# Kernel optimization log

Measured on AMD Instinct MI355X. Metric: run time of the kernel, lower is better.

Reference implementation:

```python
import jax, jax.numpy as jnp
import numpy as np

H = 512  # hidden_dim


def setup_inputs() -> dict:
    key = jax.random.key(0)
    ks = jax.random.split(key, 16)
    inp = {
        "state": jax.random.normal(ks[0], (64,), jnp.float32),
        "p_action": jax.random.normal(ks[1], (4,), jnp.float32),
        "p_reward": jax.random.normal(ks[2], (1,), jnp.float32),
        "timestep": jax.random.normal(ks[3], (1,), jnp.float32),
        "cue": jax.random.normal(ks[4], (H,), jnp.float32),
        "mem_keys": jax.random.normal(ks[5], (100000, H), jnp.float32),
        "mem_vals": jax.random.normal(ks[6], (100000, H), jnp.float32),
        "Wx": jax.random.normal(ks[7], (5 * H, 70), jnp.float32) * 0.05,
        "Wh": jax.random.normal(ks[8], (5 * H, H), jnp.float32) * 0.05,
        "b": jax.random.normal(ks[9], (5 * H,), jnp.float32) * 0.05,
        "actor_w": jax.random.normal(ks[10], (4, H), jnp.float32) * 0.01,
        "actor_b": jnp.zeros((4,), jnp.float32),
        "critic_w": jax.random.normal(ks[11], (1, H), jnp.float32),
        "critic_b": jnp.zeros((1,), jnp.float32),
        "h0": jax.random.normal(ks[12], (H,), jnp.float32),
        "c0": jax.random.normal(ks[13], (H,), jnp.float32),
    }
    return inp


def reference(state, p_action, p_reward, timestep, cue, mem_keys, mem_vals,
              Wx, Wh, b, actor_w, actor_b, critic_w, critic_b, h0, c0):
    # ---- DND.get_memory: l2-kernel softmax-weighted read over memory bank ----
    # sims[n] = -||K[n] - cue||^2 ; m_t = softmax(sims) @ V
    sims = -jnp.sum((mem_keys - cue[None, :]) ** 2, axis=1)  # [N]
    w = jax.nn.softmax(sims)                                  # [N]
    m_t = w @ mem_vals                                        # [H]

    # ---- EpLSTMCell (DND-LSTM cell: gates f,i,o,r + candidate) ----
    x_t = jnp.concatenate([state, p_action, p_reward, timestep])  # [70]
    preact = Wx @ x_t + Wh @ h0 + b                               # [5H]
    gates = jax.nn.sigmoid(preact[: 4 * H])
    f_t, i_t, o_t, r_t = jnp.split(gates, 4)
    c_hat = jnp.tanh(preact[4 * H:])
    c_t = f_t * c0 + i_t * c_hat + r_t * m_t
    h_t = o_t * jnp.tanh(c_t)

    # ---- actor / critic heads ----
    action_dist = jax.nn.softmax(actor_w @ h_t + actor_b)
    value_estimate = critic_w @ h_t + critic_b
    return (action_dist, value_estimate, h_t, c_t)
```

## Files before the change

kernel.cpp:

```cpp
#include <hip/hip_runtime.h>
#include <math.h>

#define HDIM 512
#define NROWS 100000
#define NBLK_A 2048
#define K_CAP 1024

constexpr int SIMS_OFF   = 0;
constexpr int BMIN_OFF   = NROWS;
constexpr int CNTL_OFF   = BMIN_OFF + NBLK_A;
constexpr int CAND_OFF   = CNTL_OFF + NBLK_A;
constexpr int PREACT_OFF = CAND_OFF + NBLK_A * 128;

__device__ __forceinline__ float wave_sum(float v) {
    #pragma unroll
    for (int off = 32; off; off >>= 1) v += __shfl_xor(v, off);
    return v;
}
__device__ __forceinline__ float wave_min(float v) {
    #pragma unroll
    for (int off = 32; off; off >>= 1) v = fminf(v, __shfl_xor(v, off));
    return v;
}
__device__ __forceinline__ float d2sum(float4 a, float4 c) {
    float d, s;
    d = a.x - c.x; s  = d * d;
    d = a.y - c.y; s += d * d;
    d = a.z - c.z; s += d * d;
    d = a.w - c.w; s += d * d;
    return s;
}

__global__ __launch_bounds__(256)
void kA(const float* __restrict__ state, const float* __restrict__ pa,
        const float* __restrict__ pr, const float* __restrict__ ts,
        const float* __restrict__ cue, const float* __restrict__ K,
        const float* __restrict__ Wx, const float* __restrict__ Wh,
        const float* __restrict__ b, const float* __restrict__ h0,
        float* __restrict__ ws) {
    const int lane = threadIdx.x & 63;
    const int wib  = threadIdx.x >> 6;
    const int gw   = blockIdx.x * 4 + wib;
    const int nw   = NBLK_A * 4;

    if (gw < 5 * HDIM) {
        const int row = gw;
        float x0 = state[lane];
        float x1 = 0.f;
        if      (lane < 4)  x1 = pa[lane];
        else if (lane == 4) x1 = pr[0];
        else if (lane == 5) x1 = ts[0];

        const float4* h04 = (const float4*)h0;
        const float4  hA = h04[lane], hB = h04[64 + lane];
        const float4* wh4 = (const float4*)(Wh + (size_t)row * HDIM);
        const float4 a0 = wh4[lane], a1 = wh4[64 + lane];
        float acc = a0.x*hA.x + a0.y*hA.y + a0.z*hA.z + a0.w*hA.w
                  + a1.x*hB.x + a1.y*hB.y + a1.z*hB.z + a1.w*hB.w;
        const float* wxr = Wx + (size_t)row * 70;
        acc += wxr[lane] * x0;
        if (lane < 6) acc += wxr[64 + lane] * x1;
        acc = wave_sum(acc);
        if (lane == 0) ws[PREACT_OFF + row] = acc + b[row];
    }

    const float4* c4 = (const float4*)cue;
    const float4 cA = c4[lane], cB = c4[64 + lane];
    float minss = INFINITY;

    const float4 inf4 = make_float4(INFINITY, INFINITY, INFINITY, INFINITY);
    float4 r0 = inf4, r1 = inf4, r2 = inf4, r3 = inf4;
    int it = 0;

    const int NG = NROWS / 4;
    for (int g = gw; g < NG; g += nw) {
        const int n = g * 4;
        const float* r = K + (size_t)n * HDIM;
        const float4* p0 = (const float4*)(r);
        const float4* p1 = (const float4*)(r + HDIM);
        const float4* p2 = (const float4*)(r + 2 * HDIM);
        const float4* p3 = (const float4*)(r + 3 * HDIM);
        const float4 a0 = p0[lane], b0 = p0[64 + lane];
        const float4 a1 = p1[lane], b1 = p1[64 + lane];
        const float4 a2 = p2[lane], b2 = p2[64 + lane];
        const float4 a3 = p3[lane], b3 = p3[64 + lane];
        float s0 = d2sum(a0, cA) + d2sum(b0, cB);
        float s1 = d2sum(a1, cA) + d2sum(b1, cB);
        float s2 = d2sum(a2, cA) + d2sum(b2, cB);
        float s3 = d2sum(a3, cA) + d2sum(b3, cB);
        #pragma unroll
        for (int off = 32; off; off >>= 1) {
            s0 += __shfl_xor(s0, off);
            s1 += __shfl_xor(s1, off);
            s2 += __shfl_xor(s2, off);
            s3 += __shfl_xor(s3, off);
        }
        if (lane == 0) {
            *(float4*)&ws[SIMS_OFF + n] = make_float4(-s0, -s1, -s2, -s3);
        }
        const float4 res = make_float4(s0, s1, s2, s3);
        if      (it == 0) r0 = res;
        else if (it == 1) r1 = res;
        else if (it == 2) r2 = res;
        else              r3 = res;
        ++it;
        minss = fminf(fminf(minss, s0), fminf(fminf(s1, s2), s3));
    }

    minss = wave_min(minss);
    __shared__ float smin[4];
    __shared__ int   wcnt[4];
    if (lane == 0) smin[wib] = minss;
    __syncthreads();
    const float bminv = fminf(fminf(smin[0], smin[1]),
                              fminf(smin[2], smin[3]));
    if (threadIdx.x == 0) ws[BMIN_OFF + blockIdx.x] = bminv;
    const float thr = bminv + 30.0f;

    const int qi = lane >> 2, qj = lane & 3;
    const float4 rq = (qi == 0) ? r0 : (qi == 1) ? r1 : (qi == 2) ? r2 : r3;
    const float v  = (qj == 0) ? rq.x : (qj == 1) ? rq.y : (qj == 2) ? rq.z : rq.w;
    const bool valid = (lane < 16) && (gw + qi * nw < NG);
    const bool ok    = valid && (v <= thr);
    const unsigned long long mask = __ballot(ok);
    const int cnt = (int)__popcll(mask);
    if (lane == 0) wcnt[wib] = cnt;
    __syncthreads();
    int woff = 0;
    #pragma unroll
    for (int w = 0; w < 4; w++) if (w < wib) woff += wcnt[w];
    if (ok) {
        const int pos = (int)__popcll(mask & ((1ull << lane) - 1ull));
        const int row = (gw + qi * nw) * 4 + qj;
        float2* cand = (float2*)(ws + CAND_OFF);
        cand[(blockIdx.x << 6) + woff + pos] = make_float2(v, __int_as_float(row));
    }
    if (threadIdx.x == 0)
        ((int*)ws)[CNTL_OFF + blockIdx.x] = wcnt[0] + wcnt[1] + wcnt[2] + wcnt[3];
}

__global__ __launch_bounds__(1024)
void kB(const float* __restrict__ V, const float* __restrict__ c0,
        const float* __restrict__ aw, const float* __restrict__ ab,
        const float* __restrict__ cw, const float* __restrict__ cb,
        float* __restrict__ ws, float* __restrict__ out) {
    const int t    = threadIdx.x;
    const int lane = t & 63;
    const int wib  = t >> 6;

    __shared__ float sred[16];
    __shared__ int   wtot[16];
    __shared__ int   stot;
    __shared__ float surv_s[K_CAP];
    __shared__ int   surv_n[K_CAP];
    __shared__ float sden;
    __shared__ float hl[HDIM];
    __shared__ float logits[4];

    float mn = fminf(ws[BMIN_OFF + t], ws[BMIN_OFF + 1024 + t]);
    mn = wave_min(mn);
    if (lane == 0) sred[wib] = mn;
    __syncthreads();
    float smin = sred[0];
    #pragma unroll
    for (int w = 1; w < 16; w++) smin = fminf(smin, sred[w]);
    const float thr = smin + 30.0f;

    const int*    cnts = (const int*)ws + CNTL_OFF;
    const float2* cand = (const float2*)(ws + CAND_OFF);

    int mycnt = 0;
    #pragma unroll
    for (int L = 0; L < 2; L++) {
        const int bidx = 2 * t + L;
        const int c = cnts[bidx];
        for (int e = 0; e < c; e++)
            if (cand[(bidx << 6) + e].x <= thr) mycnt++;
    }
    int inc = mycnt;
    #pragma unroll
    for (int off = 1; off < 64; off <<= 1) {
        const int v = __shfl_up(inc, off);
        if (lane >= off) inc += v;
    }
    if (lane == 63) wtot[wib] = inc;
    __syncthreads();
    int base = 0;
    #pragma unroll
    for (int w = 0; w < 16; w++) if (w < wib) base += wtot[w];
    int off = base + inc - mycnt;
    #pragma unroll
    for (int L = 0; L < 2; L++) {
        const int bidx = 2 * t + L;
        const int c = cnts[bidx];
        for (int e = 0; e < c; e++) {
            const float2 ce = cand[(bidx << 6) + e];
            if (ce.x <= thr) {
                if (off < K_CAP) {
                    surv_s[off] = ce.x;
                    surv_n[off] = __float_as_int(ce.y);
                }
                off++;
            }
        }
    }
    if (t == 1023) stot = off;
    __syncthreads();
    const int tot = (stot < K_CAP) ? stot : K_CAP;

    if (t == 0) {
        float den = 0.f;
        for (int i = 0; i < tot; i++) {
            const float e = expf(smin - surv_s[i]);
            surv_s[i] = e;
            den += e;
        }
        sden = den;
    }
    __syncthreads();
    const float inv_den = 1.f / sden;

    if (t < HDIM) {
        float m = 0.f;
        for (int i = 0; i < tot; i++)
            m += surv_s[i] * V[(size_t)surv_n[i] * HDIM + t];
        m *= inv_den;

        const float pf = ws[PREACT_OFF + t];
        const float pi = ws[PREACT_OFF + HDIM + t];
        const float po = ws[PREACT_OFF + 2*HDIM + t];
        const float prg= ws[PREACT_OFF + 3*HDIM + t];
        const float pc = ws[PREACT_OFF + 4*HDIM + t];
        const float f_t = 1.f / (1.f + expf(-pf));
        const float i_t = 1.f / (1.f + expf(-pi));
        const float o_t = 1.f / (1.f + expf(-po));
        const float r_t = 1.f / (1.f + expf(-prg));
        const float chat = tanhf(pc);
        const float ct = f_t * c0[t] + i_t * chat + r_t * m;
        const float ht = o_t * tanhf(ct);
        out[517 + t] = ct;
        out[5 + t]   = ht;
        hl[t] = ht;
    }
    __syncthreads();

    if (wib < 4) {
        float acc = 0.f;
        #pragma unroll
        for (int j = 0; j < HDIM; j += 64)
            acc += aw[wib * HDIM + j + lane] * hl[j + lane];
        acc = wave_sum(acc);
        if (lane == 0) logits[wib] = acc + ab[wib];
    }
    if (wib == 4) {
        float acc = 0.f;
        #pragma unroll
        for (int j = 0; j < HDIM; j += 64)
            acc += cw[j + lane] * hl[j + lane];
        acc = wave_sum(acc);
        if (lane == 0) out[4] = acc + cb[0];
    }
    __syncthreads();

    if (t == 0) {
        const float mx = fmaxf(fmaxf(logits[0], logits[1]),
                               fmaxf(logits[2], logits[3]));
        const float e0 = expf(logits[0] - mx), e1 = expf(logits[1] - mx);
        const float e2 = expf(logits[2] - mx), e3 = expf(logits[3] - mx);
        const float inv = 1.f / (e0 + e1 + e2 + e3);
        out[0] = e0 * inv; out[1] = e1 * inv;
        out[2] = e2 * inv; out[3] = e3 * inv;
    }
}

extern "C" void kernel_launch(void* const* d_in, const int* in_sizes, int n_in,
                              void* d_out, int out_size, void* d_ws, size_t ws_size,
                              hipStream_t stream) {
    const float* state  = (const float*)d_in[0];
    const float* pa     = (const float*)d_in[1];
    const float* pr     = (const float*)d_in[2];
    const float* ts     = (const float*)d_in[3];
    const float* cue    = (const float*)d_in[4];
    const float* keys   = (const float*)d_in[5];
    const float* vals   = (const float*)d_in[6];
    const float* Wx     = (const float*)d_in[7];
    const float* Wh     = (const float*)d_in[8];
    const float* b      = (const float*)d_in[9];
    const float* aw     = (const float*)d_in[10];
    const float* ab     = (const float*)d_in[11];
    const float* cw     = (const float*)d_in[12];
    const float* cb     = (const float*)d_in[13];
    const float* h0     = (const float*)d_in[14];
    const float* c0     = (const float*)d_in[15];
    float* ws  = (float*)d_ws;
    float* out = (float*)d_out;

    kA<<<NBLK_A, 256, 0, stream>>>(state, pa, pr, ts, cue, keys, Wx, Wh, b, h0, ws);
    kB<<<1, 1024, 0, stream>>>(vals, c0, aw, ab, cw, cb, ws, out);
}
```

Baseline: 54.57 us.

## Replace per-block candidate lists with global atomic min and compacted list

The first kernel now reduces the global minimum distance with an atomicMin on the float bits and appends threshold survivors to one compacted global list via a per-wave atomicAdd. It no longer writes the full sims array. The single-block second kernel drops its 2048-block scan and instead filters the compact list with shared-memory atomics, then insertion-sorts the survivors by row so the summation order is deterministic. This costs two memsets, global atomics, and a serial sort on one thread.

```diff
diff --git a/kernel.cpp b/kernel.cpp
--- a/kernel.cpp
+++ b/kernel.cpp
@@ -5,12 +5,12 @@
 #define NROWS 100000
 #define NBLK_A 2048
 #define K_CAP 1024
-
-constexpr int SIMS_OFF   = 0;
-constexpr int BMIN_OFF   = NROWS;
-constexpr int CNTL_OFF   = BMIN_OFF + NBLK_A;
-constexpr int CAND_OFF   = CNTL_OFF + NBLK_A;
-constexpr int PREACT_OFF = CAND_OFF + NBLK_A * 128;
+#define LISTCAP 65536
+
+constexpr int SMIN_OFF   = 0;
+constexpr int LCNT_OFF   = 1;
+constexpr int PREACT_OFF = 16;
+constexpr int LIST_OFF   = PREACT_OFF + 5 * HDIM;
 
 __device__ __forceinline__ float wave_sum(float v) {
     #pragma unroll
@@ -95,9 +95,6 @@
             s2 += __shfl_xor(s2, off);
             s3 += __shfl_xor(s3, off);
         }
-        if (lane == 0) {
-            *(float4*)&ws[SIMS_OFF + n] = make_float4(-s0, -s1, -s2, -s3);
-        }
         const float4 res = make_float4(s0, s1, s2, s3);
         if      (it == 0) r0 = res;
         else if (it == 1) r1 = res;
@@ -108,38 +105,39 @@
     }
 
     minss = wave_min(minss);
-    __shared__ float smin[4];
-    __shared__ int   wcnt[4];
-    if (lane == 0) smin[wib] = minss;
-    __syncthreads();
-    const float bminv = fminf(fminf(smin[0], smin[1]),
-                              fminf(smin[2], smin[3]));
-    if (threadIdx.x == 0) ws[BMIN_OFF + blockIdx.x] = bminv;
-    const float thr = bminv + 30.0f;
+    __shared__ float smin4[4];
+    if (lane == 0) smin4[wib] = minss;
+    __syncthreads();
+    const float bminv = fminf(fminf(smin4[0], smin4[1]),
+                              fminf(smin4[2], smin4[3]));
+    if (threadIdx.x == 0)
+        atomicMin((int*)ws + SMIN_OFF, __float_as_int(bminv));
+    const float thr0 = bminv + 30.0f;
 
     const int qi = lane >> 2, qj = lane & 3;
     const float4 rq = (qi == 0) ? r0 : (qi == 1) ? r1 : (qi == 2) ? r2 : r3;
-    const float v  = (qj == 0) ? rq.x : (qj == 1) ? rq.y : (qj == 2) ? rq.z : rq.w;
+    const float v  = (qj == 0) ? rq.x : (qj == 1) ? rq.y
+                   : (qj == 2) ? rq.z : rq.w;
     const bool valid = (lane < 16) && (gw + qi * nw < NG);
-    const bool ok    = valid && (v <= thr);
+    const bool ok    = valid && (v <= thr0);
     const unsigned long long mask = __ballot(ok);
     const int cnt = (int)__popcll(mask);
-    if (lane == 0) wcnt[wib] = cnt;
-    __syncthreads();
-    int woff = 0;
-    #pragma unroll
-    for (int w = 0; w < 4; w++) if (w < wib) woff += wcnt[w];
+    int base = 0;
+    if (lane == 0 && cnt > 0)
+        base = atomicAdd((int*)ws + LCNT_OFF, cnt);
+    base = __shfl(base, 0);
     if (ok) {
         const int pos = (int)__popcll(mask & ((1ull << lane) - 1ull));
-        const int row = (gw + qi * nw) * 4 + qj;
-        float2* cand = (float2*)(ws + CAND_OFF);
-        cand[(blockIdx.x << 6) + woff + pos] = make_float2(v, __int_as_float(row));
-    }
-    if (threadIdx.x == 0)
-        ((int*)ws)[CNTL_OFF + blockIdx.x] = wcnt[0] + wcnt[1] + wcnt[2] + wcnt[3];
-}
-
-__global__ __launch_bounds__(1024)
+        const int idx = base + pos;
+        if (idx < LISTCAP) {
+            const int row = (gw + qi * nw) * 4 + qj;
+            float2* list = (float2*)(ws + LIST_OFF);
+            list[idx] = make_float2(v, __int_as_float(row));
+        }
+    }
+}
+
+__global__ __launch_bounds__(512)
 void kB(const float* __restrict__ V, const float* __restrict__ c0,
         const float* __restrict__ aw, const float* __restrict__ ab,
         const float* __restrict__ cw, const float* __restrict__ cb,
@@ -148,69 +146,50 @@
     const int lane = t & 63;
     const int wib  = t >> 6;
 
-    __shared__ float sred[16];
-    __shared__ int   wtot[16];
-    __shared__ int   stot;
     __shared__ float surv_s[K_CAP];
     __shared__ int   surv_n[K_CAP];
+    __shared__ int   lcnt;
     __shared__ float sden;
     __shared__ float hl[HDIM];
     __shared__ float logits[4];
 
-    float mn = fminf(ws[BMIN_OFF + t], ws[BMIN_OFF + 1024 + t]);
-    mn = wave_min(mn);
-    if (lane == 0) sred[wib] = mn;
-    __syncthreads();
-    float smin = sred[0];
-    #pragma unroll
-    for (int w = 1; w < 16; w++) smin = fminf(smin, sred[w]);
-    const float thr = smin + 30.0f;
-
-    const int*    cnts = (const int*)ws + CNTL_OFF;
-    const float2* cand = (const float2*)(ws + CAND_OFF);
-
-    int mycnt = 0;
-    #pragma unroll
-    for (int L = 0; L < 2; L++) {
-        const int bidx = 2 * t + L;
-        const int c = cnts[bidx];
-        for (int e = 0; e < c; e++)
-            if (cand[(bidx << 6) + e].x <= thr) mycnt++;
-    }
-    int inc = mycnt;
-    #pragma unroll
-    for (int off = 1; off < 64; off <<= 1) {
-        const int v = __shfl_up(inc, off);
-        if (lane >= off) inc += v;
-    }
-    if (lane == 63) wtot[wib] = inc;
-    __syncthreads();
-    int base = 0;
-    #pragma unroll
-    for (int w = 0; w < 16; w++) if (w < wib) base += wtot[w];
-    int off = base + inc - mycnt;
-    #pragma unroll
-    for (int L = 0; L < 2; L++) {
-        const int bidx = 2 * t + L;
-        const int c = cnts[bidx];
-        for (int e = 0; e < c; e++) {
-            const float2 ce = cand[(bidx << 6) + e];
-            if (ce.x <= thr) {
-                if (off < K_CAP) {
-                    surv_s[off] = ce.x;
-                    surv_n[off] = __float_as_int(ce.y);
-                }
-                off++;
+    if (t == 0) lcnt = 0;
+    __syncthreads();
+
+    const float smin = __int_as_float(((const int*)ws)[SMIN_OFF]);
+    const float thr  = smin + 30.0f;
+    int total = ((const int*)ws)[LCNT_OFF];
+    if (total > LISTCAP) total = LISTCAP;
+    const float2* list = (const float2*)(ws + LIST_OFF);
+
+    for (int i = t; i < total; i += 512) {
+        const float2 e = list[i];
+        if (e.x <= thr) {
+            const int s = atomicAdd(&lcnt, 1);
+            if (s < K_CAP) {
+                surv_s[s] = e.x;
+                surv_n[s] = __float_as_int(e.y);
             }
         }
     }
-    if (t == 1023) stot = off;
-    __syncthreads();
-    const int tot = (stot < K_CAP) ? stot : K_CAP;
+    __syncthreads();
+    const int m = (lcnt < K_CAP) ? lcnt : K_CAP;
 
     if (t == 0) {
+        for (int i = 1; i < m; i++) {
+            const float ks = surv_s[i];
+            const int   kn = surv_n[i];
+            int j = i - 1;
+            while (j >= 0 && surv_n[j] > kn) {
+                surv_s[j + 1] = surv_s[j];
+                surv_n[j + 1] = surv_n[j];
+                j--;
+            }
+            surv_s[j + 1] = ks;
+            surv_n[j + 1] = kn;
+        }
         float den = 0.f;
-        for (int i = 0; i < tot; i++) {
+        for (int i = 0; i < m; i++) {
             const float e = expf(smin - surv_s[i]);
             surv_s[i] = e;
             den += e;
@@ -220,11 +199,11 @@
     __syncthreads();
     const float inv_den = 1.f / sden;
 
-    if (t < HDIM) {
-        float m = 0.f;
-        for (int i = 0; i < tot; i++)
-            m += surv_s[i] * V[(size_t)surv_n[i] * HDIM + t];
-        m *= inv_den;
+    {
+        float mm = 0.f;
+        for (int i = 0; i < m; i++)
+            mm += surv_s[i] * V[(size_t)surv_n[i] * HDIM + t];
+        mm *= inv_den;
 
         const float pf = ws[PREACT_OFF + t];
         const float pi = ws[PREACT_OFF + HDIM + t];
@@ -236,7 +215,7 @@
         const float o_t = 1.f / (1.f + expf(-po));
         const float r_t = 1.f / (1.f + expf(-prg));
         const float chat = tanhf(pc);
-        const float ct = f_t * c0[t] + i_t * chat + r_t * m;
+        const float ct = f_t * c0[t] + i_t * chat + r_t * mm;
         const float ht = o_t * tanhf(ct);
         out[517 + t] = ct;
         out[5 + t]   = ht;
@@ -295,6 +274,10 @@
     float* ws  = (float*)d_ws;
     float* out = (float*)d_out;
 
-    kA<<<NBLK_A, 256, 0, stream>>>(state, pa, pr, ts, cue, keys, Wx, Wh, b, h0, ws);
-    kB<<<1, 1024, 0, stream>>>(vals, c0, aw, ab, cw, cb, ws, out);
-}
+    (void)hipMemsetAsync((int*)ws + SMIN_OFF, 0x7F, sizeof(int), stream);
+    (void)hipMemsetAsync((int*)ws + LCNT_OFF, 0x00, sizeof(int), stream);
+
+    kA<<<NBLK_A, 256, 0, stream>>>(state, pa, pr, ts, cue, keys,
+                                   Wx, Wh, b, h0, ws);
+    kB<<<1, 512, 0, stream>>>(vals, c0, aw, ab, cw, cb, ws, out);
+}
```

After: 114.1 us. 109% more time.
